# Performance work log

Hardware: AMD Instinct MI355X
Metric: run time of the kernel (lower is better)

## Reference

```python
import jax, jax.numpy as jnp
import numpy as np

STRIDE = 4
VOX = float(STRIDE + 1)  # voxel_size = [stride+1, stride+1]
IMG_W, IMG_H = 640.0, 480.0
N, F, E, FE, B = 300000, 64, 2400000, 8, 8


def setup_inputs() -> dict:
    key = jax.random.key(0)
    ks = jax.random.split(key, 6)
    x = jax.random.normal(ks[0], (N, F), jnp.float32)
    t = jax.random.uniform(ks[1], (N, 1), jnp.float32) * 100.0
    xy = jax.random.uniform(ks[2], (N, 2), jnp.float32) * jnp.array([IMG_W, IMG_H], jnp.float32)
    pos = jnp.concatenate([t, xy], axis=1)  # [N,3] = (time, x, y)
    batch = jnp.sort(jax.random.randint(ks[3], (N,), 0, B, jnp.int32))
    edge_index = jax.random.randint(ks[4], (2, E), 0, N, jnp.int32)
    edge_attr = jax.random.normal(ks[5], (E, FE), jnp.float32)
    return {"x": x, "pos": pos, "batch": batch, "edge_index": edge_index, "edge_attr": edge_attr}


def _forward(x, pos, batch, edge_index, edge_attr):
    n = x.shape[0]
    e = edge_index.shape[1]
    # ---- voxel_grid on pos[:,1:3] with per-sample batch separation ----
    p = pos[:, 1:3]
    start = jnp.min(p, axis=0)
    end = jnp.max(p, axis=0)
    coords = jnp.floor((p - start) / VOX).astype(jnp.int32)            # [N,2]
    dims = (jnp.floor((end - start) / VOX) + 1.0).astype(jnp.int32)    # [2]
    raw = batch * (dims[0] * dims[1]) + coords[:, 0] * dims[1] + coords[:, 1]
    # ---- consecutive_cluster: relabel voxel ids to 0..C-1 ----
    fill = jnp.iinfo(jnp.int32).max
    uniq, cluster = jnp.unique(raw, return_inverse=True, size=n, fill_value=fill)
    n_clusters = jnp.sum(uniq != fill)
    # ---- node pooling: scatter-max x, scatter-mean pos, batch per cluster ----
    new_x = jax.ops.segment_max(x, cluster, num_segments=n)
    cnt = jax.ops.segment_sum(jnp.ones((n,), pos.dtype), cluster, num_segments=n)
    new_pos = jax.ops.segment_sum(pos, cluster, num_segments=n) / jnp.maximum(cnt, 1.0)[:, None]
    new_batch = jax.ops.segment_max(batch, cluster, num_segments=n)
    valid = jnp.arange(n) < n_clusters
    new_x = jnp.where(valid[:, None], new_x, 0.0)
    new_pos = jnp.where(valid[:, None], new_pos, 0.0)
    new_batch = jnp.where(valid, new_batch, -1)
    # pos[:,1:3] //= scale (float floor-division, as torch // on float tensors)
    new_pos = new_pos.at[:, 1:3].set(jnp.floor(new_pos[:, 1:3] / float(STRIDE)))
    # ---- pool_edge: remap to cluster ids, drop self-loops, coalesce (sum attr) ----
    cs = cluster[edge_index[0]]
    cd = cluster[edge_index[1]]
    loop = cs == cd
    cs = jnp.where(loop, n, cs)   # sentinel group for self-loops (sorts last)
    cd = jnp.where(loop, n, cd)
    order = jnp.lexsort((cd, cs))
    cs_s, cd_s, ea_s = cs[order], cd[order], edge_attr[order]
    newg = jnp.concatenate([jnp.ones((1,), bool), (cs_s[1:] != cs_s[:-1]) | (cd_s[1:] != cd_s[:-1])])
    gid = jnp.cumsum(newg.astype(jnp.int32)) - 1
    src = jax.ops.segment_max(cs_s, gid, num_segments=e)
    dst = jax.ops.segment_max(cd_s, gid, num_segments=e)
    new_ea = jax.ops.segment_sum(ea_s, gid, num_segments=e)
    evalid = (jnp.arange(e) <= gid[-1]) & (src >= 0) & (src < n)
    new_edge_index = jnp.stack([jnp.where(evalid, src, -1), jnp.where(evalid, dst, -1)])
    new_ea = jnp.where(evalid[:, None], new_ea, 0.0)
    return new_x, new_pos, new_batch, new_edge_index, new_ea


def reference(x, pos, batch, edge_index, edge_attr):
    return _forward(x, pos, batch, edge_index, edge_attr)
```

## Files before the change

kernel.cpp:

```cpp
#include <hip/hip_runtime.h>

#define NN 300000
#define FF 64
#define EE 2400000
#define FEA 8
#define RAWCAP 131072
#define NBUCK 4096
#define SUBB 32
#define NSB 512
#define TILE ((EE + NSB - 1) / NSB)
#define CAP 2048

typedef unsigned long long ull;

__device__ __forceinline__ unsigned fenc(float f) {
  unsigned b = __float_as_uint(f);
  return (b & 0x80000000u) ? ~b : (b | 0x80000000u);
}
__device__ __forceinline__ float fdec(unsigned e) {
  unsigned b = (e & 0x80000000u) ? (e ^ 0x80000000u) : ~e;
  return __uint_as_float(b);
}

__global__ void init_hdr_k(unsigned* hdr) {
  if (threadIdx.x == 0) {
    hdr[0] = 0xFFFFFFFFu; hdr[1] = 0xFFFFFFFFu;
    hdr[2] = 0u;          hdr[3] = 0u;
    hdr[13] = 0u;
  }
}

__global__ void minmax_k(const float* __restrict__ pos, unsigned* hdr) {
  __shared__ unsigned red[4][4];
  int t = blockIdx.x * blockDim.x + threadIdx.x;
  float mnx = 1e30f, mny = 1e30f, mxx = -1e30f, mxy = -1e30f;
  for (int i = t; i < NN; i += gridDim.x * blockDim.x) {
    float px = pos[i * 3 + 1], py = pos[i * 3 + 2];
    mnx = fminf(mnx, px); mny = fminf(mny, py);
    mxx = fmaxf(mxx, px); mxy = fmaxf(mxy, py);
  }
  for (int o = 1; o < 64; o <<= 1) {
    mnx = fminf(mnx, __shfl_xor(mnx, o));
    mny = fminf(mny, __shfl_xor(mny, o));
    mxx = fmaxf(mxx, __shfl_xor(mxx, o));
    mxy = fmaxf(mxy, __shfl_xor(mxy, o));
  }
  int wid = threadIdx.x >> 6;
  if ((threadIdx.x & 63) == 0) {
    red[wid][0] = fenc(mnx); red[wid][1] = fenc(mny);
    red[wid][2] = fenc(mxx); red[wid][3] = fenc(mxy);
  }
  __syncthreads();
  if (threadIdx.x == 0) {
    unsigned a0 = red[0][0], a1 = red[0][1], a2 = red[0][2], a3 = red[0][3];
    for (int k = 1; k < 4; k++) {
      a0 = min(a0, red[k][0]); a1 = min(a1, red[k][1]);
      a2 = max(a2, red[k][2]); a3 = max(a3, red[k][3]);
    }
    atomicMin(&hdr[0], a0); atomicMin(&hdr[1], a1);
    atomicMax(&hdr[2], a2); atomicMax(&hdr[3], a3);
  }
}

__global__ void dims_k(unsigned* hdr) {
  if (threadIdx.x == 0 && blockIdx.x == 0) {
    float mnx = fdec(hdr[0]), mny = fdec(hdr[1]);
    float mxx = fdec(hdr[2]), mxy = fdec(hdr[3]);
    int d0 = (int)(floorf((mxx - mnx) / 5.0f) + 1.0f);
    int d1 = (int)(floorf((mxy - mny) / 5.0f) + 1.0f);
    hdr[4] = (unsigned)d0;
    hdr[5] = (unsigned)d1;
    ((float*)hdr)[6] = mnx;
    ((float*)hdr)[7] = mny;
  }
}

__global__ void raw_k(const float* __restrict__ pos, const int* __restrict__ batch,
                      const unsigned* __restrict__ hdr, int* __restrict__ cluster,
                      unsigned* __restrict__ flags) {
  int i = blockIdx.x * blockDim.x + threadIdx.x;
  if (i >= NN) return;
  float mnx = ((const float*)hdr)[6], mny = ((const float*)hdr)[7];
  int d0 = (int)hdr[4], d1 = (int)hdr[5];
  int c0 = (int)floorf((pos[i * 3 + 1] - mnx) / 5.0f);
  int c1 = (int)floorf((pos[i * 3 + 2] - mny) / 5.0f);
  int raw = batch[i] * (d0 * d1) + c0 * d1 + c1;
  cluster[i] = raw;
  flags[raw] = 1u;
}

__global__ void __launch_bounds__(256)
scan_lb_k(const unsigned* __restrict__ in, unsigned* __restrict__ out, int ntot,
          unsigned* __restrict__ total_out, ull* __restrict__ desc, int nb) {
  __shared__ unsigned sc[256];
  __shared__ unsigned s_pref;
  int bid = blockIdx.x;
  int base = bid * 1024 + threadIdx.x * 4;
  unsigned v[4]; unsigned s = 0;
#pragma unroll
  for (int k = 0; k < 4; k++) {
    int i = base + k;
    v[k] = (i < ntot) ? in[i] : 0u;
    s += v[k];
  }
  sc[threadIdx.x] = s;
  __syncthreads();
  unsigned xv = s;
  for (int o = 1; o < 256; o <<= 1) {
    unsigned y = (threadIdx.x >= o) ? sc[threadIdx.x - o] : 0u;
    __syncthreads();
    xv += y;
    sc[threadIdx.x] = xv;
    __syncthreads();
  }
  unsigned btot = sc[255];
  if (threadIdx.x == 0) {
    unsigned ex = 0;
    if (bid == 0) {
      atomicExch(&desc[0], (2ULL << 32) | (ull)btot);
    } else {
      atomicExch(&desc[bid], (1ULL << 32) | (ull)btot);
      int p = bid - 1;
      while (true) {
        ull d = atomicAdd(&desc[p], 0ULL);
        unsigned fl = (unsigned)(d >> 32);
        if (fl == 2u) { ex += (unsigned)d; break; }
        if (fl == 1u) { ex += (unsigned)d; --p; }
      }
      atomicExch(&desc[bid], (2ULL << 32) | (ull)(ex + btot));
    }
    s_pref = ex;
    if (total_out && bid == nb - 1) *total_out = ex + btot;
  }
  __syncthreads();
  unsigned run = s_pref + xv - s;
#pragma unroll
  for (int k = 0; k < 4; k++) {
    int i = base + k;
    if (i < ntot) out[i] = run;
    run += v[k];
  }
}

__global__ void node_cnt_k(const unsigned* __restrict__ rank, int* __restrict__ cluster,
                           unsigned* __restrict__ cnt) {
  int i = blockIdx.x * blockDim.x + threadIdx.x;
  if (i >= NN) return;
  unsigned cl = rank[cluster[i]];
  unsigned r = atomicAdd(&cnt[cl], 1u);
  cluster[i] = (int)((r << 17) | cl);
}

__global__ void node_scatter_k(const int* __restrict__ cluster,
                               const unsigned* __restrict__ node_off,
                               int* __restrict__ nlist) {
  int i = blockIdx.x * blockDim.x + threadIdx.x;
  if (i >= NN) return;
  unsigned c = (unsigned)cluster[i];
  nlist[node_off[c & 0x1FFFFu] + (c >> 17)] = i;
}

__global__ void __launch_bounds__(256)
cluster_reduce_k(const float* __restrict__ x, const float* __restrict__ pos,
                 const int* __restrict__ batch, const int* __restrict__ nlist,
                 const unsigned* __restrict__ node_off, const unsigned* __restrict__ hdr,
                 float* __restrict__ out_x, float* __restrict__ out_pos,
                 float* __restrict__ out_batch) {
  int w = (blockIdx.x * blockDim.x + threadIdx.x) >> 6;
  int nw = (gridDim.x * blockDim.x) >> 6;
  int f = threadIdx.x & 63;
  int ncl = (int)hdr[8];
  for (int c = w; c < ncl; c += nw) {
    unsigned o0 = node_off[c];
    int len = (int)(node_off[c + 1] - o0);
    float mx = -1e38f;
    long long ps = 0;
    for (int m = 0; m < len; m++) {
      int nd = nlist[o0 + m];
      mx = fmaxf(mx, x[(size_t)nd * FF + f]);
      if (f < 3) ps += (long long)llrintf(pos[nd * 3 + f] * 65536.0f);
    }
    out_x[(size_t)c * FF + f] = mx;
    if (f < 3) {
      float v = (float)((double)ps / 65536.0 / (double)len);
      if (f > 0) v = floorf(v / 4.0f);
      out_pos[c * 3 + f] = v;
    }
    if (f == 63) out_batch[c] = (float)batch[nlist[o0]];
  }
}

__global__ void node_tail_k(const unsigned* __restrict__ hdr,
                            float* __restrict__ out_x, float* __restrict__ out_pos,
                            float* __restrict__ out_batch) {
  int ncl = (int)hdr[8];
  int total = (NN - ncl) * FF;
  for (int i = blockIdx.x * blockDim.x + threadIdx.x; i < total;
       i += gridDim.x * blockDim.x) {
    int r = ncl + (i >> 6), f = i & 63;
    out_x[(size_t)r * FF + f] = 0.0f;
    if (f < 3) out_pos[r * 3 + f] = 0.0f;
    if (f == 0) out_batch[r] = -1.0f;
  }
}


__global__ void __launch_bounds__(256)
coarse_cnt_k(const int* __restrict__ ei, const int* __restrict__ cluster,
             unsigned* __restrict__ mat) {
  __shared__ unsigned h[NBUCK];
  for (int i = threadIdx.x; i < NBUCK; i += 256) h[i] = 0u;
  __syncthreads();
  int t0 = blockIdx.x * TILE;
  for (int k = threadIdx.x; k < TILE; k += 256) {
    int t = t0 + k;
    if (t >= EE) break;
    unsigned s = (unsigned)cluster[ei[t]] & 0x1FFFFu;
    unsigned d = (unsigned)cluster[ei[EE + t]] & 0x1FFFFu;
    if (s != d) atomicAdd(&h[s >> 5], 1u);
  }
  __syncthreads();
  for (int i = threadIdx.x; i < NBUCK; i += 256)
    mat[(size_t)blockIdx.x * NBUCK + i] = h[i];
}

__global__ void transpose_k(const unsigned* __restrict__ mat, unsigned* __restrict__ matT) {
  int f = blockIdx.x * blockDim.x + threadIdx.x;
  if (f >= NSB * NBUCK) return;
  int cb = f / NSB, blk = f - cb * NSB;
  matT[f] = mat[(size_t)blk * NBUCK + cb];
}

__global__ void __launch_bounds__(256)
coarse_scatter_k(const int* __restrict__ ei, const int* __restrict__ cluster,
                 const unsigned* __restrict__ matT, ull* __restrict__ keys) {
  __shared__ unsigned cur[NBUCK];
  for (int i = threadIdx.x; i < NBUCK; i += 256)
    cur[i] = matT[(size_t)i * NSB + blockIdx.x];
  __syncthreads();
  int t0 = blockIdx.x * TILE;
  for (int k = threadIdx.x; k < TILE; k += 256) {
    int t = t0 + k;
    if (t >= EE) break;
    unsigned s = (unsigned)cluster[ei[t]] & 0x1FFFFu;
    unsigned d = (unsigned)cluster[ei[EE + t]] & 0x1FFFFu;
    if (s == d) continue;
    unsigned p = atomicAdd(&cur[s >> 5], 1u);
    keys[p] = ((ull)(s & 31u) << 39) | ((ull)d << 22) | (unsigned)t;
  }
}

__global__ void __launch_bounds__(256)
grp_emit_k(const ull* __restrict__ keys, const unsigned* __restrict__ matT,
           unsigned* __restrict__ hdr, ull* __restrict__ desc,
           const float* __restrict__ ea,
           float* __restrict__ out_src, float* __restrict__ out_dst,
           float* __restrict__ out_ea) {
  __shared__ ull sk2[CAP];
  __shared__ unsigned char hflag[CAP];
  __shared__ unsigned h[SUBB], pre[SUBB + 1], cur[SUBB], hc[SUBB], hpre[SUBB];
  __shared__ unsigned sG, sBase, sCnt, sBid;
  int tid = threadIdx.x;
  if (tid == 0) sBid = atomicAdd(&hdr[13], 1u);
  __syncthreads();
  int cb = (int)sBid;
  unsigned start = matT[(size_t)cb * NSB];
  unsigned end = (cb == NBUCK - 1) ? hdr[11] : matT[(size_t)(cb + 1) * NSB];
  int len = (int)(end - start);
  bool lds = (len <= CAP);
  unsigned G = 0;

  if (len > 0 && lds) {
    if (tid < SUBB) h[tid] = 0u;
    __syncthreads();
    for (int i = tid; i < len; i += 256)
      atomicAdd(&h[(unsigned)(keys[start + i] >> 39) & (SUBB - 1u)], 1u);
    __syncthreads();
    if (tid == 0) {
      unsigned run = 0;
      for (int j = 0; j < SUBB; j++) { pre[j] = run; run += h[j]; }
      pre[SUBB] = run;
    }
    __syncthreads();
    if (tid < SUBB) cur[tid] = pre[tid];
    __syncthreads();
    for (int i = tid; i < len; i += 256) {
      ull v = keys[start + i];
      unsigned j = (unsigned)(v >> 39) & (SUBB - 1u);
      sk2[atomicAdd(&cur[j], 1u)] = v;
    }
    __syncthreads();
    for (int i = tid; i < len; i += 256) {
      ull v = sk2[i];
      unsigned j = (unsigned)(v >> 39) & (SUBB - 1u);
      unsigned key22 = (unsigned)(v >> 22);
      bool head = true;
      for (int q = (int)pre[j]; q < i; ++q)
        if ((unsigned)(sk2[q] >> 22) == key22) { head = false; break; }
      hflag[i] = head ? 1 : 0;
    }
    __syncthreads();
    if (tid < SUBB) {
      unsigned c = 0;
      for (unsigned q = pre[tid]; q < pre[tid + 1]; ++q) c += hflag[q];
      hc[tid] = c;
    }
    __syncthreads();
    if (tid == 0) {
      unsigned run = 0;
      for (int j = 0; j < SUBB; j++) { hpre[j] = run; run += hc[j]; }
      sG = run;
    }
    __syncthreads();
    G = sG;
  } else if (len > 0) {
    if (tid == 0) sG = 0;
    __syncthreads();
    for (int j = 0; j < SUBB; j++) {
      if (tid == 0) sCnt = 0;
      __syncthreads();
      for (int i = tid; i < len; i += 256) {
        ull v = keys[start + i];
        if (((unsigned)(v >> 39) & (SUBB - 1u)) == (unsigned)j) {
          unsigned p = atomicAdd(&sCnt, 1u);
          if (p < CAP) sk2[p] = v;
        }
      }
      __syncthreads();
      int sl = min((int)sCnt, CAP);
      for (int i = tid; i < sl; i += 256) {
        unsigned key22 = (unsigned)(sk2[i] >> 22);
        bool head = true;
        for (int q = 0; q < i; ++q)
          if ((unsigned)(sk2[q] >> 22) == key22) { head = false; break; }
        hflag[i] = head ? 1 : 0;
      }
      __syncthreads();
      if (tid == 0) {
        unsigned c = 0;
        for (int q = 0; q < sl; ++q) c += hflag[q];
        hc[j] = c; hpre[j] = sG; sG += c;
      }
      __syncthreads();
    }
    G = sG;
  }

  if (tid == 0) {
    unsigned ex = 0;
    if (cb == 0) {
      atomicExch(&desc[0], (2ULL << 32) | (ull)G);
    } else {
      atomicExch(&desc[cb], (1ULL << 32) | (ull)G);
      int p = cb - 1;
      while (true) {
        ull d = atomicAdd(&desc[p], 0ULL);
        unsigned fl = (unsigned)(d >> 32);
        if (fl == 2u) { ex += (unsigned)d; break; }
        if (fl == 1u) { ex += (unsigned)d; --p; }
      }
      atomicExch(&desc[cb], (2ULL << 32) | (ull)(ex + G));
    }
    sBase = ex;
    if (cb == NBUCK - 1) hdr[12] = ex + G;
  }
  __syncthreads();
  unsigned base = sBase;
  if (len <= 0) return;

  if (lds) {
    for (int i = tid; i < len; i += 256) {
      if (!hflag[i]) continue;
      ull v = sk2[i];
      unsigned j = (unsigned)(v >> 39) & (SUBB - 1u);
      unsigned key22 = (unsigned)(v >> 22);
      unsigned r = 0;
      for (unsigned q = pre[j]; q < pre[j + 1]; ++q)
        if (hflag[q] && (unsigned)(sk2[q] >> 22) < key22) r++;
      unsigned eid = (unsigned)(v & 0x3FFFFFULL);
      const float4* p4 = (const float4*)&ea[(size_t)eid * FEA];
      float4 a0 = p4[0], a1 = p4[1];
      bool single = (hc[j] == pre[j + 1] - pre[j]);
      if (!single) {
        for (unsigned q = pre[j]; q < pre[j + 1]; ++q) {
          if (q == (unsigned)i) continue;
          ull v2 = sk2[q];
          if ((unsigned)(v2 >> 22) == key22) {
            const float4* q4 = (const float4*)&ea[(size_t)(v2 & 0x3FFFFFULL) * FEA];
            float4 b0 = q4[0], b1 = q4[1];
            a0.x += b0.x; a0.y += b0.y; a0.z += b0.z; a0.w += b0.w;
            a1.x += b1.x; a1.y += b1.y; a1.z += b1.z; a1.w += b1.w;
          }
        }
      }
      unsigned row = base + hpre[j] + r;
      out_src[row] = (float)(cb * SUBB + (int)j);
      out_dst[row] = (float)(key22 & 0x1FFFFu);
      float4* o = (float4*)&out_ea[(size_t)row * FEA];
      o[0] = a0; o[1] = a1;
    }
  } else {
    for (int j = 0; j < SUBB; j++) {
      if (tid == 0) sCnt = 0;
      __syncthreads();
      for (int i = tid; i < len; i += 256) {
        ull v = keys[start + i];
        if (((unsigned)(v >> 39) & (SUBB - 1u)) == (unsigned)j) {
          unsigned p = atomicAdd(&sCnt, 1u);
          if (p < CAP) sk2[p] = v;
        }
      }
      __syncthreads();
      int sl = min((int)sCnt, CAP);
      for (int i = tid; i < sl; i += 256) {
        unsigned key22 = (unsigned)(sk2[i] >> 22);
        bool head = true;
        for (int q = 0; q < i; ++q)
          if ((unsigned)(sk2[q] >> 22) == key22) { head = false; break; }
        hflag[i] = head ? 1 : 0;
      }
      __syncthreads();
      for (int i = tid; i < sl; i += 256) {
        if (!hflag[i]) continue;
        ull v = sk2[i];
        unsigned key22 = (unsigned)(v >> 22);
        unsigned r = 0;
        for (int q = 0; q < sl; ++q)
          if (hflag[q] && (unsigned)(sk2[q] >> 22) < key22) r++;
        const float4* p4 = (const float4*)&ea[(size_t)(v & 0x3FFFFFULL) * FEA];
        float4 a0 = p4[0], a1 = p4[1];
        bool single = (hc[j] == (unsigned)sl);
        if (!single) {
          for (int q = 0; q < sl; ++q) {
            if (q == i) continue;
            ull v2 = sk2[q];
            if ((unsigned)(v2 >> 22) == key22) {
              const float4* q4 = (const float4*)&ea[(size_t)(v2 & 0x3FFFFFULL) * FEA];
              float4 b0 = q4[0], b1 = q4[1];
              a0.x += b0.x; a0.y += b0.y; a0.z += b0.z; a0.w += b0.w;
              a1.x += b1.x; a1.y += b1.y; a1.z += b1.z; a1.w += b1.w;
            }
          }
        }
        unsigned row = base + hpre[j] + r;
        out_src[row] = (float)(cb * SUBB + j);
        out_dst[row] = (float)(key22 & 0x1FFFFu);
        float4* o = (float4*)&out_ea[(size_t)row * FEA];
        o[0] = a0; o[1] = a1;
      }
      __syncthreads();
    }
  }
}

__global__ void tail_fill_k(const unsigned* __restrict__ hdr,
                            float* __restrict__ out_src, float* __restrict__ out_dst,
                            float* __restrict__ out_ea) {
  int T = (int)hdr[12];
  for (int t = T + blockIdx.x * blockDim.x + threadIdx.x; t < EE;
       t += gridDim.x * blockDim.x) {
    out_src[t] = -1.0f;
    out_dst[t] = -1.0f;
    float4 z = make_float4(0.f, 0.f, 0.f, 0.f);
    float4* o = (float4*)&out_ea[(size_t)t * FEA];
    o[0] = z; o[1] = z;
  }
}

extern "C" void kernel_launch(void* const* d_in, const int* in_sizes, int n_in,
                              void* d_out, int out_size, void* d_ws, size_t ws_size,
                              hipStream_t stream) {
  const float* x   = (const float*)d_in[0];
  const float* pos = (const float*)d_in[1];
  const int* batch = (const int*)d_in[2];
  const int* ei    = (const int*)d_in[3];
  const float* ea  = (const float*)d_in[4];
  float* out = (float*)d_out;

  const size_t OX = 0;
  const size_t OP = (size_t)NN * FF;
  const size_t OB = OP + (size_t)NN * 3;
  const size_t OE = OB + (size_t)NN;
  const size_t OA = OE + (size_t)2 * EE;

  char* w = (char*)d_ws;
  size_t woff = 0;
  auto alloc = [&](size_t bytes) -> void* {
    void* p = w + woff;
    woff += (bytes + 255) & ~(size_t)255;
    return p;
  };
  unsigned* rank    = (unsigned*)alloc((size_t)RAWCAP * 4);
  unsigned* cnt     = (unsigned*)alloc((size_t)(NN + 1) * 4);
  ull* desc0        = (ull*)alloc(4096 * 8);
  ull* desc1        = (ull*)alloc(4096 * 8);
  ull* desc2        = (ull*)alloc(4096 * 8);
  ull* desc3        = (ull*)alloc(4096 * 8);
  size_t zero_bytes = woff;
  int* cluster      = (int*)alloc((size_t)NN * 4);
  int* nlist        = (int*)alloc((size_t)NN * 4);
  unsigned* node_off= (unsigned*)alloc((size_t)(NN + 2) * 4);
  unsigned* mat     = (unsigned*)alloc((size_t)NSB * NBUCK * 4);
  unsigned* matT    = (unsigned*)alloc((size_t)NSB * NBUCK * 4);
  unsigned* hdr     = (unsigned*)alloc(256);
  ull* keys         = (ull*)alloc((size_t)EE * 8);

  hipMemsetAsync(d_ws, 0, zero_bytes, stream);

  init_hdr_k<<<1, 64, 0, stream>>>(hdr);
  minmax_k<<<128, 256, 0, stream>>>(pos, hdr);
  dims_k<<<1, 64, 0, stream>>>(hdr);
  raw_k<<<(NN + 255) / 256, 256, 0, stream>>>(pos, batch, hdr, cluster, rank);

  auto scan1 = [&](const unsigned* in_, unsigned* out_, int ntot,
                   unsigned* total_out, ull* d_) {
    int nb = (ntot + 1023) / 1024;
    scan_lb_k<<<nb, 256, 0, stream>>>(in_, out_, ntot, total_out, d_, nb);
  };
  scan1(rank, rank, RAWCAP, hdr + 8, desc0);

  node_cnt_k<<<(NN + 255) / 256, 256, 0, stream>>>(rank, cluster, cnt);
  scan1(cnt, node_off, NN + 1, nullptr, desc1);
  node_scatter_k<<<(NN + 255) / 256, 256, 0, stream>>>(cluster, node_off, nlist);
  cluster_reduce_k<<<2048, 256, 0, stream>>>(x, pos, batch, nlist, node_off, hdr,
                                             out + OX, out + OP, out + OB);
  node_tail_k<<<2048, 256, 0, stream>>>(hdr, out + OX, out + OP, out + OB);

  coarse_cnt_k<<<NSB, 256, 0, stream>>>(ei, cluster, mat);
  transpose_k<<<(NSB * NBUCK + 255) / 256, 256, 0, stream>>>(mat, matT);
  scan1(matT, matT, NSB * NBUCK, hdr + 11, desc2);
  coarse_scatter_k<<<NSB, 256, 0, stream>>>(ei, cluster, matT, keys);
  grp_emit_k<<<NBUCK, 256, 0, stream>>>(keys, matT, hdr, desc3, ea,
                                        out + OE, out + OE + EE, out + OA);
  tail_fill_k<<<512, 256, 0, stream>>>(hdr, out + OE, out + OE + EE, out + OA);
}
```

Measured before the change: 452.7 us.

## Assign one wavefront per sub-bucket and dedup edges with cross-lane ops

In the edge grouping and emit kernel, each 64-lane wavefront now handles whole sub-buckets instead of threads striding over all keys. For sub-buckets of at most 64 edges, head detection, rank computation and attribute summation use readlane, ballot and shuffles in registers rather than repeated LDS scans. The head mask is kept in shared memory for the emit phase. Larger sub-buckets fall back to the old LDS loops, which are now written branch-free, and the extra shuffle work may cost more when duplicates are rare.

```diff
diff --git a/kernel.cpp b/kernel.cpp
--- a/kernel.cpp
+++ b/kernel.cpp
@@ -258,9 +258,11 @@
            float* __restrict__ out_ea) {
   __shared__ ull sk2[CAP];
   __shared__ unsigned char hflag[CAP];
+  __shared__ ull Mmask[SUBB];
   __shared__ unsigned h[SUBB], pre[SUBB + 1], cur[SUBB], hc[SUBB], hpre[SUBB];
   __shared__ unsigned sG, sBase, sCnt, sBid;
   int tid = threadIdx.x;
+  int wid = tid >> 6, lane = tid & 63;
   if (tid == 0) sBid = atomicAdd(&hdr[13], 1u);
   __syncthreads();
   int cb = (int)sBid;
@@ -286,24 +288,35 @@
     __syncthreads();
     for (int i = tid; i < len; i += 256) {
       ull v = keys[start + i];
-      unsigned j = (unsigned)(v >> 39) & (SUBB - 1u);
-      sk2[atomicAdd(&cur[j], 1u)] = v;
-    }
-    __syncthreads();
-    for (int i = tid; i < len; i += 256) {
-      ull v = sk2[i];
-      unsigned j = (unsigned)(v >> 39) & (SUBB - 1u);
-      unsigned key22 = (unsigned)(v >> 22);
-      bool head = true;
-      for (int q = (int)pre[j]; q < i; ++q)
-        if ((unsigned)(sk2[q] >> 22) == key22) { head = false; break; }
-      hflag[i] = head ? 1 : 0;
-    }
-    __syncthreads();
-    if (tid < SUBB) {
-      unsigned c = 0;
-      for (unsigned q = pre[tid]; q < pre[tid + 1]; ++q) c += hflag[q];
-      hc[tid] = c;
+      sk2[atomicAdd(&cur[(unsigned)(v >> 39) & (SUBB - 1u)], 1u)] = v;
+    }
+    __syncthreads();
+    for (int j = wid; j < SUBB; j += 4) {
+      int lj = (int)(pre[j + 1] - pre[j]);
+      if (lj == 0) { if (lane == 0) hc[j] = 0u; continue; }
+      if (lj <= 64) {
+        unsigned key22 = 0xFFFFFFFFu;
+        if (lane < lj) key22 = (unsigned)(sk2[pre[j] + lane] >> 22);
+        bool head = (lane < lj);
+        for (int q = 0; q < lj; ++q) {
+          unsigned kq = (unsigned)__builtin_amdgcn_readlane((int)key22, q);
+          if (kq == key22 && q < lane) head = false;
+        }
+        ull M = __ballot(head);
+        if (lane == 0) { hc[j] = (unsigned)__popcll(M); Mmask[j] = M; }
+      } else {
+        unsigned c = 0;
+        for (int i = (int)pre[j] + lane; i < (int)pre[j + 1]; i += 64) {
+          unsigned mine = (unsigned)(sk2[i] >> 22);
+          bool head = true;
+          for (int q = (int)pre[j]; q < i; ++q)
+            head = head && ((unsigned)(sk2[q] >> 22) != mine);
+          hflag[i] = head ? 1 : 0;
+          c += head ? 1u : 0u;
+        }
+        for (int o = 32; o > 0; o >>= 1) c += __shfl_down(c, o);
+        if (lane == 0) hc[j] = c;
+      }
     }
     __syncthreads();
     if (tid == 0) {
@@ -332,7 +345,7 @@
         unsigned key22 = (unsigned)(sk2[i] >> 22);
         bool head = true;
         for (int q = 0; q < i; ++q)
-          if ((unsigned)(sk2[q] >> 22) == key22) { head = false; break; }
+          head = head && ((unsigned)(sk2[q] >> 22) != key22);
         hflag[i] = head ? 1 : 0;
       }
       __syncthreads();
@@ -369,35 +382,81 @@
   if (len <= 0) return;
 
   if (lds) {
-    for (int i = tid; i < len; i += 256) {
-      if (!hflag[i]) continue;
-      ull v = sk2[i];
-      unsigned j = (unsigned)(v >> 39) & (SUBB - 1u);
-      unsigned key22 = (unsigned)(v >> 22);
-      unsigned r = 0;
-      for (unsigned q = pre[j]; q < pre[j + 1]; ++q)
-        if (hflag[q] && (unsigned)(sk2[q] >> 22) < key22) r++;
-      unsigned eid = (unsigned)(v & 0x3FFFFFULL);
-      const float4* p4 = (const float4*)&ea[(size_t)eid * FEA];
-      float4 a0 = p4[0], a1 = p4[1];
-      bool single = (hc[j] == pre[j + 1] - pre[j]);
-      if (!single) {
-        for (unsigned q = pre[j]; q < pre[j + 1]; ++q) {
-          if (q == (unsigned)i) continue;
-          ull v2 = sk2[q];
-          if ((unsigned)(v2 >> 22) == key22) {
-            const float4* q4 = (const float4*)&ea[(size_t)(v2 & 0x3FFFFFULL) * FEA];
-            float4 b0 = q4[0], b1 = q4[1];
-            a0.x += b0.x; a0.y += b0.y; a0.z += b0.z; a0.w += b0.w;
-            a1.x += b1.x; a1.y += b1.y; a1.z += b1.z; a1.w += b1.w;
+    for (int j = wid; j < SUBB; j += 4) {
+      int lj = (int)(pre[j + 1] - pre[j]);
+      if (lj == 0) continue;
+      if (lj <= 64) {
+        ull M = Mmask[j];
+        unsigned key22 = 0xFFFFFFFFu, eid = 0u;
+        if (lane < lj) {
+          ull v = sk2[pre[j] + lane];
+          key22 = (unsigned)(v >> 22);
+          eid = (unsigned)(v & 0x3FFFFFULL);
+        }
+        float4 v0 = make_float4(0.f, 0.f, 0.f, 0.f), v1 = v0;
+        if (lane < lj) {
+          const float4* p4 = (const float4*)&ea[(size_t)eid * FEA];
+          v0 = p4[0]; v1 = p4[1];
+        }
+        bool head = (M >> lane) & 1ULL;
+        bool allsingle = ((int)__popcll(M) == lj);
+        unsigned r = 0;
+        for (int q = 0; q < lj; ++q) {
+          unsigned kq = (unsigned)__builtin_amdgcn_readlane((int)key22, q);
+          if (((M >> q) & 1ULL) && kq < key22) r++;
+        }
+        float4 a0 = v0, a1 = v1;
+        if (!allsingle) {
+          for (int q = 0; q < lj; ++q) {
+            unsigned kq = (unsigned)__builtin_amdgcn_readlane((int)key22, q);
+            bool take = (kq == key22) && (q != lane);
+            float t0 = __shfl(v0.x, q), t1 = __shfl(v0.y, q);
+            float t2 = __shfl(v0.z, q), t3 = __shfl(v0.w, q);
+            float t4 = __shfl(v1.x, q), t5 = __shfl(v1.y, q);
+            float t6 = __shfl(v1.z, q), t7 = __shfl(v1.w, q);
+            if (take) {
+              a0.x += t0; a0.y += t1; a0.z += t2; a0.w += t3;
+              a1.x += t4; a1.y += t5; a1.z += t6; a1.w += t7;
+            }
           }
         }
-      }
-      unsigned row = base + hpre[j] + r;
-      out_src[row] = (float)(cb * SUBB + (int)j);
-      out_dst[row] = (float)(key22 & 0x1FFFFu);
-      float4* o = (float4*)&out_ea[(size_t)row * FEA];
-      o[0] = a0; o[1] = a1;
+        if (head) {
+          unsigned row = base + hpre[j] + r;
+          out_src[row] = (float)(cb * SUBB + j);
+          out_dst[row] = (float)(key22 & 0x1FFFFu);
+          float4* o = (float4*)&out_ea[(size_t)row * FEA];
+          o[0] = a0; o[1] = a1;
+        }
+      } else {
+        for (int i = (int)pre[j] + lane; i < (int)pre[j + 1]; i += 64) {
+          if (!hflag[i]) continue;
+          ull v = sk2[i];
+          unsigned key22 = (unsigned)(v >> 22);
+          unsigned r = 0;
+          for (unsigned q = pre[j]; q < pre[j + 1]; ++q)
+            r += (hflag[q] && (unsigned)(sk2[q] >> 22) < key22) ? 1u : 0u;
+          const float4* p4 = (const float4*)&ea[(size_t)(v & 0x3FFFFFULL) * FEA];
+          float4 a0 = p4[0], a1 = p4[1];
+          bool single = (hc[j] == pre[j + 1] - pre[j]);
+          if (!single) {
+            for (unsigned q = pre[j]; q < pre[j + 1]; ++q) {
+              if (q == (unsigned)i) continue;
+              ull v2 = sk2[q];
+              if ((unsigned)(v2 >> 22) == key22) {
+                const float4* q4 = (const float4*)&ea[(size_t)(v2 & 0x3FFFFFULL) * FEA];
+                float4 b0 = q4[0], b1 = q4[1];
+                a0.x += b0.x; a0.y += b0.y; a0.z += b0.z; a0.w += b0.w;
+                a1.x += b1.x; a1.y += b1.y; a1.z += b1.z; a1.w += b1.w;
+              }
+            }
+          }
+          unsigned row = base + hpre[j] + r;
+          out_src[row] = (float)(cb * SUBB + j);
+          out_dst[row] = (float)(key22 & 0x1FFFFu);
+          float4* o = (float4*)&out_ea[(size_t)row * FEA];
+          o[0] = a0; o[1] = a1;
+        }
+      }
     }
   } else {
     for (int j = 0; j < SUBB; j++) {
@@ -416,7 +475,7 @@
         unsigned key22 = (unsigned)(sk2[i] >> 22);
         bool head = true;
         for (int q = 0; q < i; ++q)
-          if ((unsigned)(sk2[q] >> 22) == key22) { head = false; break; }
+          head = head && ((unsigned)(sk2[q] >> 22) != key22);
         hflag[i] = head ? 1 : 0;
       }
       __syncthreads();
@@ -426,7 +485,7 @@
         unsigned key22 = (unsigned)(v >> 22);
         unsigned r = 0;
         for (int q = 0; q < sl; ++q)
-          if (hflag[q] && (unsigned)(sk2[q] >> 22) < key22) r++;
+          r += (hflag[q] && (unsigned)(sk2[q] >> 22) < key22) ? 1u : 0u;
         const float4* p4 = (const float4*)&ea[(size_t)(v & 0x3FFFFFULL) * FEA];
         float4 a0 = p4[0], a1 = p4[1];
         bool single = (hc[j] == (unsigned)sl);
```

After: 500.4 us. +10.5%, slower.

## Use wavefront-per-subbucket readlane scans for edge dedup head flags and ranks

Applied to the files above, without the earlier changes.

In the LDS path of the edge grouping kernel, each wavefront now owns whole sub-buckets. For sub-buckets of up to 64 keys it computes head flags and within-group ranks with readlane broadcasts and a ballot instead of per-thread LDS scans. The rank is precomputed and packed with the head bit into a 16-bit LDS array, which removes the O(n) rank loop from the emit phase. Early-exit loops elsewhere become branchless. The cost is more complex code, and only 4 wavefronts share 32 sub-buckets, which may leave the work unevenly spread across them.

```diff
diff --git a/kernel.cpp b/kernel.cpp
--- a/kernel.cpp
+++ b/kernel.cpp
@@ -257,10 +257,11 @@
            float* __restrict__ out_src, float* __restrict__ out_dst,
            float* __restrict__ out_ea) {
   __shared__ ull sk2[CAP];
-  __shared__ unsigned char hflag[CAP];
+  __shared__ unsigned short hr[CAP];
   __shared__ unsigned h[SUBB], pre[SUBB + 1], cur[SUBB], hc[SUBB], hpre[SUBB];
   __shared__ unsigned sG, sBase, sCnt, sBid;
   int tid = threadIdx.x;
+  int wid = tid >> 6, lane = tid & 63;
   if (tid == 0) sBid = atomicAdd(&hdr[13], 1u);
   __syncthreads();
   int cb = (int)sBid;
@@ -286,24 +287,50 @@
     __syncthreads();
     for (int i = tid; i < len; i += 256) {
       ull v = keys[start + i];
-      unsigned j = (unsigned)(v >> 39) & (SUBB - 1u);
-      sk2[atomicAdd(&cur[j], 1u)] = v;
-    }
-    __syncthreads();
-    for (int i = tid; i < len; i += 256) {
-      ull v = sk2[i];
-      unsigned j = (unsigned)(v >> 39) & (SUBB - 1u);
-      unsigned key22 = (unsigned)(v >> 22);
-      bool head = true;
-      for (int q = (int)pre[j]; q < i; ++q)
-        if ((unsigned)(sk2[q] >> 22) == key22) { head = false; break; }
-      hflag[i] = head ? 1 : 0;
-    }
-    __syncthreads();
-    if (tid < SUBB) {
-      unsigned c = 0;
-      for (unsigned q = pre[tid]; q < pre[tid + 1]; ++q) c += hflag[q];
-      hc[tid] = c;
+      sk2[atomicAdd(&cur[(unsigned)(v >> 39) & (SUBB - 1u)], 1u)] = v;
+    }
+    __syncthreads();
+    for (int j = wid; j < SUBB; j += 4) {
+      int lj = (int)(pre[j + 1] - pre[j]);
+      if (lj == 0) { if (lane == 0) hc[j] = 0u; continue; }
+      if (lj <= 64) {
+        unsigned key22 = 0xFFFFFFFFu;
+        if (lane < lj) key22 = (unsigned)(sk2[pre[j] + lane] >> 22);
+        bool head = (lane < lj);
+        for (int q = 0; q < lj; ++q) {
+          unsigned kq = (unsigned)__builtin_amdgcn_readlane((int)key22, q);
+          if (kq == key22 && q < lane) head = false;
+        }
+        ull M = __ballot(head);
+        unsigned r = 0;
+        for (int q = 0; q < lj; ++q) {
+          unsigned kq = (unsigned)__builtin_amdgcn_readlane((int)key22, q);
+          if (((M >> q) & 1ULL) && kq < key22) r++;
+        }
+        if (lane < lj)
+          hr[pre[j] + lane] = (unsigned short)(r | (head ? 0x8000u : 0u));
+        if (lane == 0) hc[j] = (unsigned)__popcll(M);
+      } else {
+        unsigned c = 0;
+        for (int i = (int)pre[j] + lane; i < (int)pre[j + 1]; i += 64) {
+          unsigned mine = (unsigned)(sk2[i] >> 22);
+          bool head = true;
+          for (int q = (int)pre[j]; q < i; ++q)
+            head = head && ((unsigned)(sk2[q] >> 22) != mine);
+          hr[i] = head ? 0x8000u : 0u;
+          c += head ? 1u : 0u;
+        }
+        for (int o = 32; o > 0; o >>= 1) c += __shfl_down(c, o);
+        if (lane == 0) hc[j] = c;
+        for (int i = (int)pre[j] + lane; i < (int)pre[j + 1]; i += 64) {
+          if (!(hr[i] & 0x8000u)) continue;
+          unsigned mine = (unsigned)(sk2[i] >> 22);
+          unsigned r = 0;
+          for (int q = (int)pre[j]; q < (int)pre[j + 1]; ++q)
+            r += ((hr[q] & 0x8000u) && (unsigned)(sk2[q] >> 22) < mine) ? 1u : 0u;
+          hr[i] = (unsigned short)(0x8000u | r);
+        }
+      }
     }
     __syncthreads();
     if (tid == 0) {
@@ -332,13 +359,13 @@
         unsigned key22 = (unsigned)(sk2[i] >> 22);
         bool head = true;
         for (int q = 0; q < i; ++q)
-          if ((unsigned)(sk2[q] >> 22) == key22) { head = false; break; }
-        hflag[i] = head ? 1 : 0;
+          head = head && ((unsigned)(sk2[q] >> 22) != key22);
+        hr[i] = head ? 0x8000u : 0u;
       }
       __syncthreads();
       if (tid == 0) {
         unsigned c = 0;
-        for (int q = 0; q < sl; ++q) c += hflag[q];
+        for (int q = 0; q < sl; ++q) c += (hr[q] & 0x8000u) ? 1u : 0u;
         hc[j] = c; hpre[j] = sG; sG += c;
       }
       __syncthreads();
@@ -370,18 +397,15 @@
 
   if (lds) {
     for (int i = tid; i < len; i += 256) {
-      if (!hflag[i]) continue;
+      unsigned hrv = hr[i];
+      if (!(hrv & 0x8000u)) continue;
       ull v = sk2[i];
       unsigned j = (unsigned)(v >> 39) & (SUBB - 1u);
       unsigned key22 = (unsigned)(v >> 22);
-      unsigned r = 0;
-      for (unsigned q = pre[j]; q < pre[j + 1]; ++q)
-        if (hflag[q] && (unsigned)(sk2[q] >> 22) < key22) r++;
       unsigned eid = (unsigned)(v & 0x3FFFFFULL);
       const float4* p4 = (const float4*)&ea[(size_t)eid * FEA];
       float4 a0 = p4[0], a1 = p4[1];
-      bool single = (hc[j] == pre[j + 1] - pre[j]);
-      if (!single) {
+      if (hc[j] != pre[j + 1] - pre[j]) {
         for (unsigned q = pre[j]; q < pre[j + 1]; ++q) {
           if (q == (unsigned)i) continue;
           ull v2 = sk2[q];
@@ -393,7 +417,7 @@
           }
         }
       }
-      unsigned row = base + hpre[j] + r;
+      unsigned row = base + hpre[j] + (hrv & 0x7FFFu);
       out_src[row] = (float)(cb * SUBB + (int)j);
       out_dst[row] = (float)(key22 & 0x1FFFFu);
       float4* o = (float4*)&out_ea[(size_t)row * FEA];
@@ -416,21 +440,20 @@
         unsigned key22 = (unsigned)(sk2[i] >> 22);
         bool head = true;
         for (int q = 0; q < i; ++q)
-          if ((unsigned)(sk2[q] >> 22) == key22) { head = false; break; }
-        hflag[i] = head ? 1 : 0;
+          head = head && ((unsigned)(sk2[q] >> 22) != key22);
+        hr[i] = head ? 0x8000u : 0u;
       }
       __syncthreads();
       for (int i = tid; i < sl; i += 256) {
-        if (!hflag[i]) continue;
+        if (!(hr[i] & 0x8000u)) continue;
         ull v = sk2[i];
         unsigned key22 = (unsigned)(v >> 22);
         unsigned r = 0;
         for (int q = 0; q < sl; ++q)
-          if (hflag[q] && (unsigned)(sk2[q] >> 22) < key22) r++;
+          r += ((hr[q] & 0x8000u) && (unsigned)(sk2[q] >> 22) < key22) ? 1u : 0u;
         const float4* p4 = (const float4*)&ea[(size_t)(v & 0x3FFFFFULL) * FEA];
         float4 a0 = p4[0], a1 = p4[1];
-        bool single = (hc[j] == (unsigned)sl);
-        if (!single) {
+        if (hc[j] != (unsigned)sl) {
           for (int q = 0; q < sl; ++q) {
             if (q == i) continue;
             ull v2 = sk2[q];
```

New measurement: 558.5 us. 1.23x slower.
